# Optimization experiments

Hardware: AMD Instinct MI355X
Metric: run time of the kernel (lower is better)

The kernel has to match this reference:

```python
import jax, jax.numpy as jnp
import numpy as np
from jax import lax

SIZES = (32, 64, 128, 256, 512)
STRIDES = (4, 8, 16, 32, 64)
RATIOS = (0.5, 1.0, 2.0)
LVL_HW = ((256, 256), (128, 128), (64, 64), (32, 32), (16, 16))
IMG_H = IMG_W = 1024
NMS_T = 0.7
PRE_K = 6000   # pre_nms_topk[False]
POST_K = 1000  # post_nms_topk[False]
SCALE_CLAMP = float(np.log(1000.0 / 16))


def _anchors():
    """Detectron2-style anchors, one size per level, HWA ordering (anchor innermost)."""
    out = []
    for size, stride, (H, W) in zip(SIZES, STRIDES, LVL_HW):
        r = np.asarray(RATIOS, np.float64)
        ws = np.sqrt(size * size / r)
        hs = ws * r
        cell = np.stack([-ws / 2, -hs / 2, ws / 2, hs / 2], axis=1)  # [A,4]
        yy, xx = np.meshgrid(np.arange(H) * stride, np.arange(W) * stride, indexing='ij')
        shifts = np.stack([xx, yy, xx, yy], axis=-1).reshape(-1, 1, 4)  # [HW,1,4]
        out.append(jnp.asarray((shifts + cell[None]).reshape(-1, 4), jnp.float32))  # [HW*A,4]
    return out


def _conv(x, w, b, pad):
    y = lax.conv_general_dilated(x, w, (1, 1), [(pad, pad), (pad, pad)],
                                 dimension_numbers=('NCHW', 'OIHW', 'NCHW'))
    return y + b[None, :, None, None]


def _apply_deltas(deltas, anchors):
    # deltas [N,M,4], anchors [M,4]; Box2BoxTransform weights (1,1,1,1)
    w = anchors[:, 2] - anchors[:, 0]
    h = anchors[:, 3] - anchors[:, 1]
    cx = anchors[:, 0] + 0.5 * w
    cy = anchors[:, 1] + 0.5 * h
    dx, dy = deltas[..., 0], deltas[..., 1]
    dw = jnp.minimum(deltas[..., 2], SCALE_CLAMP)
    dh = jnp.minimum(deltas[..., 3], SCALE_CLAMP)
    pcx = dx * w + cx
    pcy = dy * h + cy
    pw = jnp.exp(dw) * w
    ph = jnp.exp(dh) * h
    return jnp.stack([pcx - 0.5 * pw, pcy - 0.5 * ph, pcx + 0.5 * pw, pcy + 0.5 * ph], -1)


def _nms(boxes, scores):
    """Fixed-iteration greedy NMS: boxes [M,4], scores [M] -> (idx [POST_K], valid [POST_K])."""
    areas = (boxes[:, 2] - boxes[:, 0]) * (boxes[:, 3] - boxes[:, 1])

    def body(s, _):
        i = jnp.argmax(s)
        bs = s[i]
        bb = boxes[i]
        x1 = jnp.maximum(bb[0], boxes[:, 0])
        y1 = jnp.maximum(bb[1], boxes[:, 1])
        x2 = jnp.minimum(bb[2], boxes[:, 2])
        y2 = jnp.minimum(bb[3], boxes[:, 3])
        inter = jnp.clip(x2 - x1, 0.0) * jnp.clip(y2 - y1, 0.0)
        iou = inter / (areas[i] + areas - inter + 1e-9)
        s2 = jnp.where(iou > NMS_T, -jnp.inf, s).at[i].set(-jnp.inf)
        return s2, (i, bs > -jnp.inf)

    _, (idx, valid) = lax.scan(body, scores, None, length=POST_K)
    return idx, valid


def setup_inputs() -> dict:
    key = jax.random.key(0)
    ks = jax.random.split(key, 8)
    C = 256
    inp = {}
    for i, (H, W) in enumerate(LVL_HW):
        inp[f'f{i + 2}'] = jax.random.normal(ks[i], (2, C, H, W), jnp.float32)
    inp['conv_w'] = 0.01 * jax.random.normal(ks[5], (C, C, 3, 3), jnp.float32)
    inp['conv_b'] = jnp.zeros((C,), jnp.float32)
    inp['obj_w'] = 0.01 * jax.random.normal(ks[6], (3, C, 1, 1), jnp.float32)
    inp['obj_b'] = jnp.zeros((3,), jnp.float32)
    inp['delta_w'] = 0.01 * jax.random.normal(ks[7], (12, C, 1, 1), jnp.float32)
    inp['delta_b'] = jnp.zeros((12,), jnp.float32)
    return inp


def reference(f2, f3, f4, f5, f6, conv_w, conv_b, obj_w, obj_b, delta_w, delta_b):
    feats = [f2, f3, f4, f5, f6]
    anchors = _anchors()

    logits_l, deltas_l = [], []
    for x in feats:
        t = jax.nn.relu(_conv(x, conv_w, conv_b, 1))
        lg = _conv(t, obj_w, obj_b, 0)        # [N,A,H,W]
        dl = _conv(t, delta_w, delta_b, 0)    # [N,A*4,H,W]
        N, A, H, W = lg.shape
        logits_l.append(lg.transpose(0, 2, 3, 1).reshape(N, -1))                       # [N,HWA]
        deltas_l.append(dl.reshape(N, A, 4, H, W).transpose(0, 3, 4, 1, 2).reshape(N, -1, 4))  # [N,HWA,4]

    combined = jnp.concatenate(
        [jnp.concatenate(logits_l, 1)[..., None], jnp.concatenate(deltas_l, 1)], -1)  # [N,Atot,5]

    # decode + per-level pre-NMS top-k
    cand_b, cand_s, cand_l = [], [], []
    for lvl, (lg, dl, an) in enumerate(zip(logits_l, deltas_l, anchors)):
        props = _apply_deltas(dl, an)          # [N,HWA,4]
        k = min(PRE_K, lg.shape[1])
        vals, idx = lax.top_k(lg, k)
        cand_b.append(jnp.take_along_axis(props, idx[..., None], 1))
        cand_s.append(vals)
        cand_l.append(jnp.full(vals.shape, float(lvl), jnp.float32))
    boxes = jnp.concatenate(cand_b, 1)   # [N,M,4]
    scores = jnp.concatenate(cand_s, 1)  # [N,M]
    lvl = jnp.concatenate(cand_l, 1)

    # clip to image
    boxes = jnp.stack([boxes[..., 0].clip(0, IMG_W), boxes[..., 1].clip(0, IMG_H),
                       boxes[..., 2].clip(0, IMG_W), boxes[..., 3].clip(0, IMG_H)], -1)
    # batched NMS via per-level coordinate offset (levels never overlap)
    off_boxes = boxes + (lvl * 2000.0)[..., None]
    idx, valid = jax.vmap(_nms)(off_boxes, scores)
    keep_boxes = jnp.take_along_axis(boxes, idx[..., None], 1)   # [N,POST_K,4]
    keep_scores = jnp.take_along_axis(scores, idx, 1)            # [N,POST_K]
    return combined, keep_boxes, keep_scores, valid
```

## Files before the change

kernel.cpp:

```cpp
#include <hip/hip_runtime.h>
#include <math.h>

#define ATOT 261888
#define MCAND 21840
#define POSTK 1000
#define CMB (2*ATOT*5)
#define KB_OFF CMB
#define KS_OFF (CMB+8000)
#define KV_OFF (CMB+10000)
#define SCALE_CLAMP 4.135166556742356f
#define RCAP 4096

typedef unsigned long long u64;

#define WS_T   0
#define WS_SC  (256*65536)
#define WS_CB  (WS_SC + 2*ATOT)
#define WS_CS  (WS_CB + 2*MCAND*4)
#define WS_CTL (WS_CS + 2*MCAND)

#define C_PRE 0
#define C_KCUR 6
#define C_CNT 12
#define C_TIE 18
#define N_THRPREV 24
#define N_KEPT 26
#define N_DONE 28
#define N_SCNT 30
#define N_LAST 32
#define C_GH 40
#define C_TIEIDX (C_GH + 6*256)
#define CTL_SIZE (C_TIEIDX + 6*1024)
#define WS_WP  (WS_CTL + CTL_SIZE)

#define FT_T   0
#define FT_TSZ 22347776
#define FT_SC  22347776
#define FT_CB  (FT_SC + 2*ATOT)
#define FT_CS  (FT_CB + 2*MCAND*4)
#define FT_CTL (FT_CS + 2*MCAND)
#define FT_WP  (FT_CTL + CTL_SIZE)
#define FT_END (FT_WP + 589824)

#define NS_KEY  0
#define NS_BOX  16384
#define NS_AREA 49152
#define NS_DIAG 57344
#define NS_PSUP 73728
#define NS_KBOX 73984
#define NS_MASK 84224

__device__ const int LW[5]    = {256,128,64,32,16};
__device__ const int LM[5]    = {196608,49152,12288,3072,768};
__device__ const int LBASE[5] = {0,196608,245760,258048,261120};
__device__ const int LSTR[5]  = {4,8,16,32,64};
__device__ const int LSZ[5]   = {32,64,128,256,512};
__device__ const int CBASE[5] = {0,6000,12000,18000,21072};
__device__ const int TOFF[5]  = {0,16777216,20971520,22020096,22282240};

__device__ inline unsigned fkey(float f) {
  unsigned u = __float_as_uint(f);
  return u ^ (unsigned)(((int)u >> 31) | 0x80000000);
}
__device__ inline float unfkey(unsigned k) {
  unsigned u = (k & 0x80000000u) ? (k ^ 0x80000000u) : ~k;
  return __uint_as_float(u);
}
__device__ inline int lvl_of(int idx) {
  return idx < 6000 ? 0 : idx < 12000 ? 1 : idx < 18000 ? 2 : idx < 21072 ? 3 : 4;
}
__device__ inline float iou_f(float ax1,float ay1,float ax2,float ay2,float aar,
                              float bx1,float by1,float bx2,float by2,float bar) {
  float ix1 = fmaxf(ax1,bx1), iy1 = fmaxf(ay1,by1);
  float ix2 = fminf(ax2,bx2), iy2 = fminf(ay2,by2);
  float inter = fmaxf(ix2-ix1,0.f) * fmaxf(iy2-iy1,0.f);
  return inter / (aar + bar - inter + 1e-9f);
}

typedef _Float16 f16;
typedef _Float16 f16x2 __attribute__((ext_vector_type(2)));
typedef _Float16 f16x8 __attribute__((ext_vector_type(8)));
typedef float f32x4 __attribute__((ext_vector_type(4)));

#define MFMA16(a,b,c) __builtin_amdgcn_mfma_f32_16x16x32_f16(a,b,c,0,0,0)
#define AST 40
#define WHALF 589824

__global__ __launch_bounds__(256) void wprep_mfma(const float* __restrict__ wgt,
                                                  f16* __restrict__ wsp) {
  int o = blockIdx.x*256 + threadIdx.x;
  if (o >= WHALF) return;
  int j  = o & 7;
  int oc = (o >> 3) & 255;
  int ks = (o >> 11) & 3;
  int kc = (o >> 13) & 7;
  int t  = o >> 16;
  int ci = kc*32 + ks*8 + j;
  float v = wgt[(oc*256 + ci)*9 + t] * 2048.f;
  f16 hi = (f16)v;
  f16 lo = (f16)(v - (float)hi);
  wsp[o] = hi;
  wsp[WHALF + o] = lo;
}

#define HALO 324
#define SBUF 25920

__global__ __launch_bounds__(512,2) void conv_big(
    const float* __restrict__ f0, const float* __restrict__ f1,
    const float* __restrict__ f2, const float* __restrict__ f3,
    const float* __restrict__ f4, const f16* __restrict__ wsp,
    const float* __restrict__ bias,
    const float* __restrict__ ow, const float* __restrict__ obp,
    const float* __restrict__ dwp, const float* __restrict__ dbp,
    float* __restrict__ comb, float* __restrict__ scores) {
  __shared__ __align__(16) char SBc[103680];
  __shared__ float wHs[15][256];
  const int tid = threadIdx.x;

  int id = blockIdx.x;
  int n = (id >= 341) ? 1 : 0;
  int rem = id - n*341;
  int lvl, tile;
  if (rem < 256)      { lvl = 0; tile = rem; }
  else if (rem < 320) { lvl = 1; tile = rem - 256; }
  else if (rem < 336) { lvl = 2; tile = rem - 320; }
  else if (rem < 340) { lvl = 3; tile = rem - 336; }
  else                { lvl = 4; tile = 0; }
  const int W = LW[lvl], H = W, HW = W*W;
  const int tw = W >> 4;
  const int ty0 = tile / tw, tx0 = tile - ty0*tw;
  const int x0 = tx0*16, y0 = ty0*16;
  const int lbase = LBASE[lvl];
  const float* in = (lvl==0?f0:lvl==1?f1:lvl==2?f2:lvl==3?f3:f4) + (long)n*256*HW;

  const int wv   = tid >> 6;
  const int lane = tid & 63;
  const int l15  = lane & 15;
  const int ks   = lane >> 4;
  const int rg   = wv >> 2;
  const int cg   = wv & 3;

  for (int i = tid; i < 768; i += 512)  wHs[i>>8][i&255] = ow[i];
  for (int i = tid; i < 3072; i += 512) wHs[3+(i>>8)][i&255] = dwp[i];

  auto stage = [&](int kc, int b) {
    f16* AhB = (f16*)SBc + b*SBUF;
    f16* AlB = AhB + 12960;
    float v0r[10], v1r[10];
    #pragma unroll
    for (int it = 0; it < 10; ++it) {
      int i = tid + it*512;
      int cp = i / HALO; int p = i - cp*HALO;
      int hy = p / 18, hx = p - hy*18;
      int gy = y0 + hy - 1, gx = x0 + hx - 1;
      int cy = min(max(gy, 0), H-1), cx = min(max(gx, 0), W-1);
      const float* q = in + (long)(kc*32 + 2*cp)*HW + cy*W + cx;
      v0r[it] = q[0];
      v1r[it] = q[HW];
    }
    #pragma unroll
    for (int it = 0; it < 10; ++it) {
      int i = tid + it*512;
      int cp = i / HALO; int p = i - cp*HALO;
      int hy = p / 18, hx = p - hy*18;
      int gy = y0 + hy - 1, gx = x0 + hx - 1;
      bool okb = (gy >= 0) & (gy < H) & (gx >= 0) & (gx < W);
      float v0 = okb ? v0r[it]*2048.f : 0.f;
      float v1 = okb ? v1r[it]*2048.f : 0.f;
      f16 h0 = (f16)v0, h1 = (f16)v1;
      f16 e0 = (f16)(v0 - (float)h0), e1 = (f16)(v1 - (float)h1);
      f16x2 ph; ph[0] = h0; ph[1] = h1;
      f16x2 pl; pl[0] = e0; pl[1] = e1;
      *(f16x2*)&AhB[p*AST + 2*cp] = ph;
      *(f16x2*)&AlB[p*AST + 2*cp] = pl;
    }
    if (tid < 64) {
      int p = 5120 + tid - 15*HALO;
      int hy = p / 18, hx = p - hy*18;
      int gy = y0 + hy - 1, gx = x0 + hx - 1;
      float v0 = 0.f, v1 = 0.f;
      if (gy >= 0 && gy < H && gx >= 0 && gx < W) {
        const float* q = in + (long)(kc*32 + 30)*HW + gy*W + gx;
        v0 = q[0]*2048.f; v1 = q[HW]*2048.f;
      }
      f16 h0 = (f16)v0, h1 = (f16)v1;
      f16 e0 = (f16)(v0 - (float)h0), e1 = (f16)(v1 - (float)h1);
      f16x2 ph; ph[0] = h0; ph[1] = h1;
      f16x2 pl; pl[0] = e0; pl[1] = e1;
      *(f16x2*)&AhB[p*AST + 30] = ph;
      *(f16x2*)&AlB[p*AST + 30] = pl;
    }
  };

  const f32x4 vzero = {0.f, 0.f, 0.f, 0.f};
  f32x4 acc[8][4];
  #pragma unroll
  for (int mt = 0; mt < 8; ++mt)
    #pragma unroll
    for (int nt = 0; nt < 4; ++nt) acc[mt][nt] = vzero;

  stage(0, 0);
  __syncthreads();

  for (int kc = 0; kc < 8; ++kc) {
    const int b = kc & 1;
    if (kc < 7) stage(kc + 1, b ^ 1);
    const f16* AhB = (const f16*)SBc + b*SBUF;
    const f16* AlB = AhB + 12960;
    for (int t = 0; t < 9; ++t) {
      const int tyk = t / 3, txk = t - (t/3)*3;
      const f16* wb = wsp + (((t*8 + kc)*4 + ks)*256 + cg*64 + l15)*8;
      f16x8 Bh0 = *(const f16x8*)(wb);
      f16x8 Bh1 = *(const f16x8*)(wb + 128);
      f16x8 Bh2 = *(const f16x8*)(wb + 256);
      f16x8 Bh3 = *(const f16x8*)(wb + 384);
      f16x8 Bl0 = *(const f16x8*)(wb + WHALF);
      f16x8 Bl1 = *(const f16x8*)(wb + WHALF + 128);
      f16x8 Bl2 = *(const f16x8*)(wb + WHALF + 256);
      f16x8 Bl3 = *(const f16x8*)(wb + WHALF + 384);
      #pragma unroll
      for (int mt = 0; mt < 8; ++mt) {
        const int p = (rg*8 + mt + tyk)*18 + l15 + txk;
        f16x8 Af = *(const f16x8*)&AhB[p*AST + ks*8];
        f16x8 Ae = *(const f16x8*)&AlB[p*AST + ks*8];
        acc[mt][0] = MFMA16(Af, Bh0, acc[mt][0]);
        acc[mt][1] = MFMA16(Af, Bh1, acc[mt][1]);
        acc[mt][2] = MFMA16(Af, Bh2, acc[mt][2]);
        acc[mt][3] = MFMA16(Af, Bh3, acc[mt][3]);
        acc[mt][0] = MFMA16(Ae, Bh0, acc[mt][0]);
        acc[mt][1] = MFMA16(Ae, Bh1, acc[mt][1]);
        acc[mt][2] = MFMA16(Ae, Bh2, acc[mt][2]);
        acc[mt][3] = MFMA16(Ae, Bh3, acc[mt][3]);
        acc[mt][0] = MFMA16(Af, Bl0, acc[mt][0]);
        acc[mt][1] = MFMA16(Af, Bl1, acc[mt][1]);
        acc[mt][2] = MFMA16(Af, Bl2, acc[mt][2]);
        acc[mt][3] = MFMA16(Af, Bl3, acc[mt][3]);
      }
    }
    __syncthreads();
  }

  const float rs = 1.f / 4194304.f;
  float* part = (float*)SBc;
  float bb[4];
  #pragma unroll
  for (int nt = 0; nt < 4; ++nt) bb[nt] = bias[cg*64 + nt*16 + l15];

  #pragma unroll
  for (int mt = 0; mt < 8; ++mt) {
    f32x4 y[4];
    #pragma unroll
    for (int nt = 0; nt < 4; ++nt) {
      f32x4 a = acc[mt][nt];
      y[nt][0] = fmaxf(a[0]*rs + bb[nt], 0.f);
      y[nt][1] = fmaxf(a[1]*rs + bb[nt], 0.f);
      y[nt][2] = fmaxf(a[2]*rs + bb[nt], 0.f);
      y[nt][3] = fmaxf(a[3]*rs + bb[nt], 0.f);
    }
    #pragma unroll
    for (int j = 0; j < 15; ++j) {
      float w0 = wHs[j][cg*64 + l15];
      float w1 = wHs[j][cg*64 + 16 + l15];
      float w2 = wHs[j][cg*64 + 32 + l15];
      float w3 = wHs[j][cg*64 + 48 + l15];
      f32x4 p4;
      p4[0] = y[0][0]*w0 + y[1][0]*w1 + y[2][0]*w2 + y[3][0]*w3;
      p4[1] = y[0][1]*w0 + y[1][1]*w1 + y[2][1]*w2 + y[3][1]*w3;
      p4[2] = y[0][2]*w0 + y[1][2]*w1 + y[2][2]*w2 + y[3][2]*w3;
      p4[3] = y[0][3]*w0 + y[1][3]*w1 + y[2][3]*w2 + y[3][3]*w3;
      #pragma unroll
      for (int m = 1; m < 16; m <<= 1) {
        p4[0] += __shfl_xor(p4[0], m);
        p4[1] += __shfl_xor(p4[1], m);
        p4[2] += __shfl_xor(p4[2], m);
        p4[3] += __shfl_xor(p4[3], m);
      }
      if (l15 == 0) {
        float* pp = part + ((((cg*2 + rg)*8 + mt)*4 + ks)*15 + j)*4;
        pp[0] = p4[0]; pp[1] = p4[1]; pp[2] = p4[2]; pp[3] = p4[3];
      }
    }
  }
  __syncthreads();
  if (tid < 256) {
    int rg2 = tid >> 7, mt = (tid >> 4) & 7, xi = tid & 15;
    int k2 = xi >> 2, xj = xi & 3;
    float v[15];
    #pragma unroll
    for (int j = 0; j < 15; ++j) {
      float s = 0.f;
      #pragma unroll
      for (int c2 = 0; c2 < 4; ++c2)
        s += part[((((c2*2 + rg2)*8 + mt)*4 + k2)*15 + j)*4 + xj];
      v[j] = s;
    }
    int pos = (y0 + rg2*8 + mt)*W + x0 + xi;
    long base = (long)n*ATOT + lbase + (long)pos*3;
    #pragma unroll
    for (int a = 0; a < 3; ++a) {
      float lg = v[a] + obp[a];
      comb[(base+a)*5] = lg;
      scores[(long)n*ATOT + lbase + pos*3 + a] = lg;
      #pragma unroll
      for (int q = 0; q < 4; ++q)
        comb[(base+a)*5 + 1 + q] = v[3 + a*4 + q] + dbp[a*4+q];
    }
  }
}

__global__ __launch_bounds__(256,2) void conv_lvl_mfma(
    const float* __restrict__ in, const f16* __restrict__ wsp,
    const float* __restrict__ bias, float* __restrict__ outp, int H, int W) {
  __shared__ __align__(16) char SBc[28800];
  f16* Ah = (f16*)SBc;
  f16* Al = (f16*)(SBc + 14400);
  const int tid  = threadIdx.x;
  const int wv   = tid >> 6;
  const int lane = tid & 63;
  const int l15  = lane & 15;
  const int ks   = lane >> 4;
  const int HW   = H * W;
  const int x0 = blockIdx.x*16, y0 = blockIdx.y*8;

  const f32x4 vzero = {0.f, 0.f, 0.f, 0.f};
  f32x4 acc[8][4];
  #pragma unroll
  for (int mt = 0; mt < 8; ++mt)
    #pragma unroll
    for (int nt = 0; nt < 4; ++nt) acc[mt][nt] = vzero;

  for (int kc = 0; kc < 8; ++kc) {
    __syncthreads();
    for (int i = tid; i < 2880; i += 256) {
      int cp = i / 180; int p = i - cp*180;
      int hy = p / 18, hx = p - hy*18;
      int gy = y0 + hy - 1, gx = x0 + hx - 1;
      float v0 = 0.f, v1 = 0.f;
      if (gy >= 0 && gy < H && gx >= 0 && gx < W) {
        const float* q = in + (long)(kc*32 + 2*cp)*HW + gy*W + gx;
        v0 = q[0] * 2048.f;
        v1 = q[HW] * 2048.f;
      }
      f16 h0 = (f16)v0, h1 = (f16)v1;
      f16 e0 = (f16)(v0 - (float)h0), e1 = (f16)(v1 - (float)h1);
      f16x2 ph; ph[0] = h0; ph[1] = h1;
      f16x2 pl; pl[0] = e0; pl[1] = e1;
      *(f16x2*)&Ah[p*AST + 2*cp] = ph;
      *(f16x2*)&Al[p*AST + 2*cp] = pl;
    }
    __syncthreads();
    for (int t = 0; t < 9; ++t) {
      const int tyk = t / 3, txk = t - (t/3)*3;
      const f16* wb = wsp + (((t*8 + kc)*4 + ks)*256 + wv*64 + l15)*8;
      f16x8 Bh0 = *(const f16x8*)(wb);
      f16x8 Bh1 = *(const f16x8*)(wb + 128);
      f16x8 Bh2 = *(const f16x8*)(wb + 256);
      f16x8 Bh3 = *(const f16x8*)(wb + 384);
      f16x8 Bl0 = *(const f16x8*)(wb + WHALF);
      f16x8 Bl1 = *(const f16x8*)(wb + WHALF + 128);
      f16x8 Bl2 = *(const f16x8*)(wb + WHALF + 256);
      f16x8 Bl3 = *(const f16x8*)(wb + WHALF + 384);
      #pragma unroll
      for (int mt = 0; mt < 8; ++mt) {
        const int p = (mt + tyk)*18 + l15 + txk;
        f16x8 Af = *(const f16x8*)&Ah[p*AST + ks*8];
        f16x8 Ae = *(const f16x8*)&Al[p*AST + ks*8];
        acc[mt][0] = MFMA16(Af, Bh0, acc[mt][0]);
        acc[mt][1] = MFMA16(Af, Bh1, acc[mt][1]);
        acc[mt][2] = MFMA16(Af, Bh2, acc[mt][2]);
        acc[mt][3] = MFMA16(Af, Bh3, acc[mt][3]);
        acc[mt][0] = MFMA16(Ae, Bh0, acc[mt][0]);
        acc[mt][1] = MFMA16(Ae, Bh1, acc[mt][1]);
        acc[mt][2] = MFMA16(Ae, Bh2, acc[mt][2]);
        acc[mt][3] = MFMA16(Ae, Bh3, acc[mt][3]);
        acc[mt][0] = MFMA16(Af, Bl0, acc[mt][0]);
        acc[mt][1] = MFMA16(Af, Bl1, acc[mt][1]);
        acc[mt][2] = MFMA16(Af, Bl2, acc[mt][2]);
        acc[mt][3] = MFMA16(Af, Bl3, acc[mt][3]);
      }
    }
  }
  const float rs = 1.f / 4194304.f;
  #pragma unroll
  for (int nt = 0; nt < 4; ++nt) {
    int oc = wv*64 + nt*16 + l15;
    float bbv = bias[oc];
    #pragma unroll
    for (int mt = 0; mt < 8; ++mt) {
      f32x4 a = acc[mt][nt];
      float4 v;
      v.x = fmaxf(a[0]*rs + bbv, 0.f);
      v.y = fmaxf(a[1]*rs + bbv, 0.f);
      v.z = fmaxf(a[2]*rs + bbv, 0.f);
      v.w = fmaxf(a[3]*rs + bbv, 0.f);
      *(float4*)&outp[(long)oc*HW + (y0+mt)*W + x0 + ks*4] = v;
    }
  }
}

__global__ __launch_bounds__(256) void heads1x1(
    const float* __restrict__ t, const float* __restrict__ ow, const float* __restrict__ ob,
    const float* __restrict__ dw, const float* __restrict__ db,
    float* __restrict__ comb, float* __restrict__ scores, int HW, int lbase, int n) {
  __shared__ float wS[15][256];
  const int tid = threadIdx.x;
  for (int i = tid; i < 3*256; i += 256) wS[i>>8][i&255] = ow[i];
  for (int i = tid; i < 12*256; i += 256) wS[3+(i>>8)][i&255] = dw[i];
  __syncthreads();
  int p0 = (blockIdx.x*256 + threadIdx.x)*4;
  if (p0 >= HW) return;
  float acc[15][4] = {};
  for (int c = 0; c < 256; ++c) {
    float4 v = *(const float4*)&t[c*HW + p0];
    float vv[4] = {v.x, v.y, v.z, v.w};
    #pragma unroll
    for (int k = 0; k < 15; ++k) {
      float w = wS[k][c];
      #pragma unroll
      for (int j = 0; j < 4; ++j) acc[k][j] += w * vv[j];
    }
  }
  float obv[3]; for (int i2 = 0; i2 < 3; ++i2) obv[i2] = ob[i2];
  float dbv[12]; for (int i2 = 0; i2 < 12; ++i2) dbv[i2] = db[i2];
  for (int j = 0; j < 4; ++j) {
    int pos = p0 + j;
    long base = (long)n*ATOT + lbase + (long)pos*3;
    #pragma unroll
    for (int a = 0; a < 3; ++a) {
      float lg = acc[a][j] + obv[a];
      comb[(base+a)*5] = lg;
      scores[(long)n*ATOT + lbase + pos*3 + a] = lg;
      #pragma unroll
      for (int q = 0; q < 4; ++q)
        comb[(base+a)*5 + 1 + q] = acc[3 + a*4 + q][j] + dbv[a*4+q];
    }
  }
}

__device__ void decode_store(int n, int lvl, int idx, int slot,
                             const float* comb, float* cboxes, float* cscores) {
  int W = LW[lvl];
  int a = idx % 3; int p = idx / 3;
  int wx = p % W, hy = p / W;
  double r = (a == 0) ? 0.5 : (a == 1) ? 1.0 : 2.0;
  double sz = (double)LSZ[lvl];
  double wsd = sqrt(sz*sz/r);
  double hsd = wsd * r;
  double cxd = (double)(wx * LSTR[lvl]);
  double cyd = (double)(hy * LSTR[lvl]);
  float ax1 = (float)(cxd - 0.5*wsd), ay1 = (float)(cyd - 0.5*hsd);
  float ax2 = (float)(cxd + 0.5*wsd), ay2 = (float)(cyd + 0.5*hsd);
  float aw = ax2 - ax1, ah = ay2 - ay1;
  float acx = ax1 + 0.5f*aw, acy = ay1 + 0.5f*ah;
  long g = (long)n*ATOT + LBASE[lvl] + idx;
  const float* cm = comb + g*5;
  float sc = cm[0];
  float dx = cm[1], dy = cm[2], dwv = cm[3], dhv = cm[4];
  dwv = fminf(dwv, SCALE_CLAMP); dhv = fminf(dhv, SCALE_CLAMP);
  float pcx = __fadd_rn(__fmul_rn(dx, aw), acx);
// ... 253 lines not shown
    }
  }
}

__global__ __launch_bounds__(64) void nms_scan(
    const float* __restrict__ cscores, const float* __restrict__ cboxes,
    float* __restrict__ wt, unsigned* ctl, float* __restrict__ dout) {
  const int n = blockIdx.x;
  if (ctl[N_DONE + n]) return;
  const int lane = threadIdx.x;
  const float* cb = cboxes + (long)n*MCAND*4;
  u64* skeyG = ((u64*)(wt + NS_KEY)) + n*RCAP;
  const float* boxO  = wt + NS_BOX + n*RCAP*4;
  const float* areaG = wt + NS_AREA + n*RCAP;
  u64* mask  = ((u64*)(wt + NS_MASK)) + (long)n*RCAP*64;
  u64* diagA = ((u64*)(wt + NS_DIAG)) + n*64*64;
  u64* psupW = ((u64*)(wt + NS_PSUP)) + n*64;
  float* kbox = wt + NS_KBOX + n*1024*5;
  float* keepB = dout + KB_OFF + (long)n*4*POSTK;
  float* keepS = dout + KS_OFF + (long)n*POSTK;
  float* keepV = dout + KV_OFF + (long)n*POSTK;
  int scnt = (int)ctl[N_SCNT + n];
  int kt = (int)ctl[N_KEPT + n];
  __shared__ u64 alive[64];
  {
    int rem = scnt - lane*64;
    u64 a = rem >= 64 ? ~0ull : (rem > 0 ? ((1ull << rem) - 1ull) : 0ull);
    alive[lane] = a & ~psupW[lane];
  }
  __syncthreads();
  for (int c = 0; c < 64 && kt < POSTK; ++c) {
    u64 w64 = alive[c];
    if (!w64) continue;
    u64 diag = diagA[c*64 + lane];
    u64 kb = 0;
    while (w64) {
      int b = __ffsll(w64) - 1;
      kb |= (1ull << b);
      w64 &= ~(1ull << b);
      u64 sup = __shfl(diag, b);
      w64 &= ~sup;
      if (++kt >= POSTK) break;
    }
    alive[c] = 0;
    if ((kb >> lane) & 1) {
      int base = kt - (int)__popcll(kb);
      int pos = base + (int)__popcll(kb & ((1ull << lane) - 1ull));
      int s = c*64 + lane;
      u64 v = skeyG[s];
      int idx = (int)(~(unsigned)v);
      keepB[pos*4+0]=cb[idx*4+0]; keepB[pos*4+1]=cb[idx*4+1];
      keepB[pos*4+2]=cb[idx*4+2]; keepB[pos*4+3]=cb[idx*4+3];
      keepS[pos] = unfkey((unsigned)(v >> 32));
      keepV[pos] = 1.f;
      kbox[pos*5+0]=boxO[s*4+0]; kbox[pos*5+1]=boxO[s*4+1];
      kbox[pos*5+2]=boxO[s*4+2]; kbox[pos*5+3]=boxO[s*4+3];
      kbox[pos*5+4]=areaG[s];
    }
    __syncthreads();
    if (kb && lane > c && alive[lane]) {
      u64 acc = 0, m = kb;
      while (m) {
        int b = __ffsll(m) - 1; m &= m - 1;
        acc |= mask[(long)(c*64 + b)*64 + lane];
      }
      if (acc) alive[lane] &= ~acc;
    }
    __syncthreads();
  }
  if (lane == 0) {
    ctl[N_KEPT + n] = (unsigned)kt;
    if (kt >= POSTK || ctl[N_LAST + n]) ctl[N_DONE + n] = 1;
  }
}

__device__ inline u64 shfl_down_u64d(u64 v, int o) {
  unsigned hi = __shfl_down((unsigned)(v >> 32), o);
  unsigned lo = __shfl_down((unsigned)v, o);
  return ((u64)hi << 32) | lo;
}
__global__ __launch_bounds__(1024) void nms_fill(
    const float* __restrict__ cscores, const float* __restrict__ cboxes,
    unsigned* ctl, float* __restrict__ dout) {
  const int n = blockIdx.x;
  const int tid = threadIdx.x;
  const int lane = tid & 63;
  const int wid = tid >> 6;
  const float* sc = cscores + (long)n*MCAND;
  const float* cb = cboxes + (long)n*MCAND*4;
  float* keepB = dout + KB_OFF + (long)n*4*POSTK;
  float* keepS = dout + KS_OFF + (long)n*POSTK;
  float* keepV = dout + KV_OFF + (long)n*POSTK;
  __shared__ u64 wred[16];
  __shared__ u64 sBest;
  u64 best = 0;
  for (int i = tid; i < 6000; i += 1024) {
    u64 v = ((u64)fkey(sc[i]) << 32) | (unsigned)(~i);
    if (v > best) best = v;
  }
  for (int o = 32; o > 0; o >>= 1) {
    u64 ov = shfl_down_u64d(best, o);
    if (ov > best) best = ov;
  }
  if (lane == 0) wred[wid] = best;
  __syncthreads();
  if (tid == 0) {
    u64 b = 0;
    for (int i = 0; i < 16; ++i) if (wred[i] > b) b = wred[i];
    sBest = b;
  }
  __syncthreads();
  int kt = (int)ctl[N_KEPT + n];
  int bidx = (int)(~(unsigned)sBest);
  float b0 = cb[bidx*4+0], b1 = cb[bidx*4+1], b2 = cb[bidx*4+2], b3 = cb[bidx*4+3];
  float bsc = sc[bidx];
  for (int s2 = kt + tid; s2 < POSTK; s2 += 1024) {
    keepB[s2*4+0]=b0; keepB[s2*4+1]=b1; keepB[s2*4+2]=b2; keepB[s2*4+3]=b3;
    keepS[s2] = bsc; keepV[s2] = 0.f;
  }
}

extern "C" void kernel_launch(void* const* d_in, const int* in_sizes, int n_in,
                              void* d_out, int out_size, void* d_ws, size_t ws_size,
                              hipStream_t stream) {
  const float* feats[5];
  for (int i = 0; i < 5; ++i) feats[i] = (const float*)d_in[i];
  const float* conv_w  = (const float*)d_in[5];
  const float* conv_b  = (const float*)d_in[6];
  const float* obj_w   = (const float*)d_in[7];
  const float* obj_b   = (const float*)d_in[8];
  const float* delta_w = (const float*)d_in[9];
  const float* delta_b = (const float*)d_in[10];
  float* out = (float*)d_out;
  float* ws = (float*)d_ws;

  const bool big = ws_size >= (size_t)FT_END * 4ull;
  float *t, *scores, *cboxes, *cscores, *wp;
  unsigned* ctl;
  if (big) {
    t = ws + FT_T; scores = ws + FT_SC; cboxes = ws + FT_CB;
    cscores = ws + FT_CS; ctl = (unsigned*)(ws + FT_CTL); wp = ws + FT_WP;
  } else {
    t = ws + WS_T; scores = ws + WS_SC; cboxes = ws + WS_CB;
    cscores = ws + WS_CS; ctl = (unsigned*)(ws + WS_CTL); wp = ws + WS_WP;
  }

  static const int LWh[5]    = {256,128,64,32,16};
  static const int LBASEh[5] = {0,196608,245760,258048,261120};

  wprep_mfma<<<dim3(2304), dim3(256), 0, stream>>>(conv_w, (f16*)wp);
  init_ctl<<<dim3(1), dim3(256), 0, stream>>>(ctl);

  if (big) {
    conv_big<<<dim3(682), dim3(512), 0, stream>>>(
        feats[0], feats[1], feats[2], feats[3], feats[4], (const f16*)wp, conv_b,
        obj_w, obj_b, delta_w, delta_b, out, scores);
  } else {
    for (int n = 0; n < 2; ++n) {
      for (int lvl = 0; lvl < 5; ++lvl) {
        int H = LWh[lvl], W = LWh[lvl], HW = H*W;
        conv_lvl_mfma<<<dim3(W/16, H/8), dim3(256), 0, stream>>>(
            feats[lvl] + (long)n*256*HW, (const f16*)wp, conv_b, t, H, W);
        int hb = (HW + 1023) / 1024;
        heads1x1<<<dim3(hb), dim3(256), 0, stream>>>(
            t, obj_w, obj_b, delta_w, delta_b, out, scores, HW, LBASEh[lvl], n);
      }
    }
  }

  for (int p = 0; p < 4; ++p) {
    tk_hist<<<dim3(48,6), dim3(256), 0, stream>>>(scores, ctl, p);
    tk_pick<<<dim3(6), dim3(256), 0, stream>>>(ctl);
  }
  tk_compact<<<dim3(48,6), dim3(256), 0, stream>>>(scores, out, ctl, cboxes, cscores);
  tk_finalize<<<dim3(6), dim3(64), 0, stream>>>(out, ctl, cboxes, cscores);
  decode34<<<dim3(15,2), dim3(256), 0, stream>>>(out, cboxes, cscores);
  for (int b = 0; b < 6; ++b) {
    nms_select<<<dim3(2), dim3(1024), 0, stream>>>(cscores, cboxes, t, ctl);
    nms_matrix<<<dim3(64,2), dim3(256), 0, stream>>>(t, t, ctl);
    nms_scan<<<dim3(2), dim3(64), 0, stream>>>(cscores, cboxes, t, ctl, out);
  }
  nms_fill<<<dim3(2), dim3(1024), 0, stream>>>(cscores, cboxes, ctl, out);
}
```

Baseline: 1.656 ms.

## Widen conv_big to 1024 threads with channel-major LDS layout and deferred stage writes

Result: slower. 5.308 ms (+220.6%).

```diff
diff --git a/kernel.cpp b/kernel.cpp
--- a/kernel.cpp
+++ b/kernel.cpp
@@ -103,10 +103,11 @@
   wsp[WHALF + o] = lo;
 }
 
-#define HALO 324
-#define SBUF 25920
-
-__global__ __launch_bounds__(512,2) void conv_big(
+#define NUNIT 1296
+#define ABUF 10368
+#define SBUF2 20736
+
+__global__ __launch_bounds__(1024,4) void conv_big(
     const float* __restrict__ f0, const float* __restrict__ f1,
     const float* __restrict__ f2, const float* __restrict__ f3,
     const float* __restrict__ f4, const f16* __restrict__ wsp,
@@ -114,7 +115,7 @@
     const float* __restrict__ ow, const float* __restrict__ obp,
     const float* __restrict__ dwp, const float* __restrict__ dbp,
     float* __restrict__ comb, float* __restrict__ scores) {
-  __shared__ __align__(16) char SBc[103680];
+  __shared__ __align__(16) char SBc[82944];
   __shared__ float wHs[15][256];
   const int tid = threadIdx.x;
 
@@ -138,174 +139,164 @@
   const int lane = tid & 63;
   const int l15  = lane & 15;
   const int ks   = lane >> 4;
-  const int rg   = wv >> 2;
-  const int cg   = wv & 3;
-
-  for (int i = tid; i < 768; i += 512)  wHs[i>>8][i&255] = ow[i];
-  for (int i = tid; i < 3072; i += 512) wHs[3+(i>>8)][i&255] = dwp[i];
-
-  auto stage = [&](int kc, int b) {
-    f16* AhB = (f16*)SBc + b*SBUF;
-    f16* AlB = AhB + 12960;
-    float v0r[10], v1r[10];
+  const int rg   = wv >> 3;
+  const int cg   = wv & 7;
+
+  for (int i = tid; i < 768; i += 1024)  wHs[i>>8][i&255] = ow[i];
+  for (int i = tid; i < 3072; i += 1024) wHs[3+(i>>8)][i&255] = dwp[i];
+
+  int ks0 = tid / 324; int p0 = tid - ks0*324;
+  int hy0 = p0/18, hx0 = p0 - hy0*18;
+  int gy0 = y0 + hy0 - 1, gx0 = x0 + hx0 - 1;
+  const bool okb0 = (gy0>=0) & (gy0<H) & (gx0>=0) & (gx0<W);
+  const int boff0 = ks0*8*HW + min(max(gy0,0),H-1)*W + min(max(gx0,0),W-1);
+  const bool has1 = tid < 272;
+  int p1 = tid + 52;
+  int hy1 = p1/18, hx1 = p1 - hy1*18;
+  int gy1 = y0 + hy1 - 1, gx1 = x0 + hx1 - 1;
+  const bool okb1 = (gy1>=0) & (gy1<H) & (gx1>=0) & (gx1<W);
+  const int boff1 = 24*HW + min(max(gy1,0),H-1)*W + min(max(gx1,0),W-1);
+
+  float sv0[8], sv1[8];
+  auto stage_load = [&](int kc) {
+    const float* q = in + (size_t)(kc*32)*HW;
     #pragma unroll
-    for (int it = 0; it < 10; ++it) {
-      int i = tid + it*512;
-      int cp = i / HALO; int p = i - cp*HALO;
-      int hy = p / 18, hx = p - hy*18;
-      int gy = y0 + hy - 1, gx = x0 + hx - 1;
-      int cy = min(max(gy, 0), H-1), cx = min(max(gx, 0), W-1);
-      const float* q = in + (long)(kc*32 + 2*cp)*HW + cy*W + cx;
-      v0r[it] = q[0];
-      v1r[it] = q[HW];
-    }
+    for (int j = 0; j < 8; ++j) sv0[j] = q[boff0 + j*HW];
+    if (has1) {
+      #pragma unroll
+      for (int j = 0; j < 8; ++j) sv1[j] = q[boff1 + j*HW];
+    }
+  };
+  auto stage_write = [&](int b) {
+    f16* AhB = (f16*)SBc + b*SBUF2;
+    f16* AlB = AhB + ABUF;
+    f16x8 vh, vl;
     #pragma unroll
-    for (int it = 0; it < 10; ++it) {
-      int i = tid + it*512;
-      int cp = i / HALO; int p = i - cp*HALO;
-      int hy = p / 18, hx = p - hy*18;
-      int gy = y0 + hy - 1, gx = x0 + hx - 1;
-      bool okb = (gy >= 0) & (gy < H) & (gx >= 0) & (gx < W);
-      float v0 = okb ? v0r[it]*2048.f : 0.f;
-      float v1 = okb ? v1r[it]*2048.f : 0.f;
-      f16 h0 = (f16)v0, h1 = (f16)v1;
-      f16 e0 = (f16)(v0 - (float)h0), e1 = (f16)(v1 - (float)h1);
-      f16x2 ph; ph[0] = h0; ph[1] = h1;
-      f16x2 pl; pl[0] = e0; pl[1] = e1;
-      *(f16x2*)&AhB[p*AST + 2*cp] = ph;
-      *(f16x2*)&AlB[p*AST + 2*cp] = pl;
-    }
-    if (tid < 64) {
-      int p = 5120 + tid - 15*HALO;
-      int hy = p / 18, hx = p - hy*18;
-      int gy = y0 + hy - 1, gx = x0 + hx - 1;
-      float v0 = 0.f, v1 = 0.f;
-      if (gy >= 0 && gy < H && gx >= 0 && gx < W) {
-        const float* q = in + (long)(kc*32 + 30)*HW + gy*W + gx;
-        v0 = q[0]*2048.f; v1 = q[HW]*2048.f;
-      }
-      f16 h0 = (f16)v0, h1 = (f16)v1;
-      f16 e0 = (f16)(v0 - (float)h0), e1 = (f16)(v1 - (float)h1);
-      f16x2 ph; ph[0] = h0; ph[1] = h1;
-      f16x2 pl; pl[0] = e0; pl[1] = e1;
-      *(f16x2*)&AhB[p*AST + 30] = ph;
-      *(f16x2*)&AlB[p*AST + 30] = pl;
+    for (int j = 0; j < 8; ++j) {
+      float v = okb0 ? sv0[j]*2048.f : 0.f;
+      f16 h = (f16)v; vh[j] = h; vl[j] = (f16)(v - (float)h);
+    }
+    *(f16x8*)&AhB[tid*8] = vh;
+    *(f16x8*)&AlB[tid*8] = vl;
+    if (has1) {
+      #pragma unroll
+      for (int j = 0; j < 8; ++j) {
+        float v = okb1 ? sv1[j]*2048.f : 0.f;
+        f16 h = (f16)v; vh[j] = h; vl[j] = (f16)(v - (float)h);
+      }
+      *(f16x8*)&AhB[(1024+tid)*8] = vh;
+      *(f16x8*)&AlB[(1024+tid)*8] = vl;
     }
   };
 
   const f32x4 vzero = {0.f, 0.f, 0.f, 0.f};
-  f32x4 acc[8][4];
+  f32x4 acc[8][2];
   #pragma unroll
-  for (int mt = 0; mt < 8; ++mt)
-    #pragma unroll
-    for (int nt = 0; nt < 4; ++nt) acc[mt][nt] = vzero;
-
-  stage(0, 0);
+  for (int mt = 0; mt < 8; ++mt) { acc[mt][0] = vzero; acc[mt][1] = vzero; }
+
+  stage_load(0);
+  stage_write(0);
   __syncthreads();
 
   for (int kc = 0; kc < 8; ++kc) {
     const int b = kc & 1;
-    if (kc < 7) stage(kc + 1, b ^ 1);
-    const f16* AhB = (const f16*)SBc + b*SBUF;
-    const f16* AlB = AhB + 12960;
+    if (kc < 7) stage_load(kc + 1);
+    const f16* AhB = (const f16*)SBc + b*SBUF2;
+    const f16* AlB = AhB + ABUF;
     for (int t = 0; t < 9; ++t) {
       const int tyk = t / 3, txk = t - (t/3)*3;
-      const f16* wb = wsp + (((t*8 + kc)*4 + ks)*256 + cg*64 + l15)*8;
+      const f16* wb = wsp + (((t*8 + kc)*4 + ks)*256 + cg*32 + l15)*8;
       f16x8 Bh0 = *(const f16x8*)(wb);
       f16x8 Bh1 = *(const f16x8*)(wb + 128);
-      f16x8 Bh2 = *(const f16x8*)(wb + 256);
-      f16x8 Bh3 = *(const f16x8*)(wb + 384);
       f16x8 Bl0 = *(const f16x8*)(wb + WHALF);
       f16x8 Bl1 = *(const f16x8*)(wb + WHALF + 128);
-      f16x8 Bl2 = *(const f16x8*)(wb + WHALF + 256);
-      f16x8 Bl3 = *(const f16x8*)(wb + WHALF + 384);
       #pragma unroll
       for (int mt = 0; mt < 8; ++mt) {
         const int p = (rg*8 + mt + tyk)*18 + l15 + txk;
-        f16x8 Af = *(const f16x8*)&AhB[p*AST + ks*8];
-        f16x8 Ae = *(const f16x8*)&AlB[p*AST + ks*8];
+        f16x8 Af = *(const f16x8*)&AhB[(ks*324 + p)*8];
+        f16x8 Ae = *(const f16x8*)&AlB[(ks*324 + p)*8];
         acc[mt][0] = MFMA16(Af, Bh0, acc[mt][0]);
         acc[mt][1] = MFMA16(Af, Bh1, acc[mt][1]);
-        acc[mt][2] = MFMA16(Af, Bh2, acc[mt][2]);
-        acc[mt][3] = MFMA16(Af, Bh3, acc[mt][3]);
         acc[mt][0] = MFMA16(Ae, Bh0, acc[mt][0]);
         acc[mt][1] = MFMA16(Ae, Bh1, acc[mt][1]);
-        acc[mt][2] = MFMA16(Ae, Bh2, acc[mt][2]);
-        acc[mt][3] = MFMA16(Ae, Bh3, acc[mt][3]);
         acc[mt][0] = MFMA16(Af, Bl0, acc[mt][0]);
         acc[mt][1] = MFMA16(Af, Bl1, acc[mt][1]);
-        acc[mt][2] = MFMA16(Af, Bl2, acc[mt][2]);
-        acc[mt][3] = MFMA16(Af, Bl3, acc[mt][3]);
-      }
-    }
+      }
+    }
+    if (kc < 7) stage_write(b ^ 1);
     __syncthreads();
   }
 
   const float rs = 1.f / 4194304.f;
-  float* part = (float*)SBc;
-  float bb[4];
-  #pragma unroll
-  for (int nt = 0; nt < 4; ++nt) bb[nt] = bias[cg*64 + nt*16 + l15];
-
+  float bb0 = bias[cg*32 + l15], bb1 = bias[cg*32 + 16 + l15];
   #pragma unroll
   for (int mt = 0; mt < 8; ++mt) {
-    f32x4 y[4];
+    f32x4 a0 = acc[mt][0], a1 = acc[mt][1];
     #pragma unroll
-    for (int nt = 0; nt < 4; ++nt) {
-      f32x4 a = acc[mt][nt];
-      y[nt][0] = fmaxf(a[0]*rs + bb[nt], 0.f);
-      y[nt][1] = fmaxf(a[1]*rs + bb[nt], 0.f);
-      y[nt][2] = fmaxf(a[2]*rs + bb[nt], 0.f);
-      y[nt][3] = fmaxf(a[3]*rs + bb[nt], 0.f);
-    }
+    for (int i = 0; i < 4; ++i) {
+      a0[i] = fmaxf(a0[i]*rs + bb0, 0.f);
+      a1[i] = fmaxf(a1[i]*rs + bb1, 0.f);
+    }
+    acc[mt][0] = a0; acc[mt][1] = a1;
+  }
+
+  float* part = (float*)SBc;
+  #pragma unroll
+  for (int h = 0; h < 2; ++h) {
+    const int jb = h*8;
     #pragma unroll
-    for (int j = 0; j < 15; ++j) {
-      float w0 = wHs[j][cg*64 + l15];
-      float w1 = wHs[j][cg*64 + 16 + l15];
-      float w2 = wHs[j][cg*64 + 32 + l15];
-      float w3 = wHs[j][cg*64 + 48 + l15];
-      f32x4 p4;
-      p4[0] = y[0][0]*w0 + y[1][0]*w1 + y[2][0]*w2 + y[3][0]*w3;
-      p4[1] = y[0][1]*w0 + y[1][1]*w1 + y[2][1]*w2 + y[3][1]*w3;
-      p4[2] = y[0][2]*w0 + y[1][2]*w1 + y[2][2]*w2 + y[3][2]*w3;
-      p4[3] = y[0][3]*w0 + y[1][3]*w1 + y[2][3]*w2 + y[3][3]*w3;
+    for (int mt = 0; mt < 8; ++mt) {
       #pragma unroll
-      for (int m = 1; m < 16; m <<= 1) {
-        p4[0] += __shfl_xor(p4[0], m);
-        p4[1] += __shfl_xor(p4[1], m);
-        p4[2] += __shfl_xor(p4[2], m);
-        p4[3] += __shfl_xor(p4[3], m);
-      }
-      if (l15 == 0) {
-        float* pp = part + ((((cg*2 + rg)*8 + mt)*4 + ks)*15 + j)*4;
-        pp[0] = p4[0]; pp[1] = p4[1]; pp[2] = p4[2]; pp[3] = p4[3];
-      }
-    }
-  }
-  __syncthreads();
-  if (tid < 256) {
-    int rg2 = tid >> 7, mt = (tid >> 4) & 7, xi = tid & 15;
-    int k2 = xi >> 2, xj = xi & 3;
-    float v[15];
-    #pragma unroll
-    for (int j = 0; j < 15; ++j) {
-      float s = 0.f;
+      for (int jj = 0; jj < 8; ++jj) {
+        const int j = jb + jj;
+        if (j < 15) {
+          float w0 = wHs[j][cg*32 + l15];
+          float w1 = wHs[j][cg*32 + 16 + l15];
+          f32x4 p4;
+          #pragma unroll
+          for (int i = 0; i < 4; ++i)
+            p4[i] = acc[mt][0][i]*w0 + acc[mt][1][i]*w1;
+          #pragma unroll
+          for (int m = 1; m < 16; m <<= 1) {
+            p4[0] += __shfl_xor(p4[0], m);
+            p4[1] += __shfl_xor(p4[1], m);
+            p4[2] += __shfl_xor(p4[2], m);
+            p4[3] += __shfl_xor(p4[3], m);
+          }
+          if (l15 == 0) {
+            float* pp = part + ((((cg*2 + rg)*8 + mt)*4 + ks)*8 + jj)*4;
+            pp[0] = p4[0]; pp[1] = p4[1]; pp[2] = p4[2]; pp[3] = p4[3];
+          }
+        }
+      }
+    }
+    __syncthreads();
+    if (tid < 256) {
+      int row16 = tid >> 4, xi = tid & 15;
+      int rg2 = row16 >> 3, mt = row16 & 7;
+      int k2 = xi >> 2, xj = xi & 3;
+      int pos = (y0 + rg2*8 + mt)*W + x0 + xi;
+      long base = (long)n*ATOT + lbase + (long)pos*3;
       #pragma unroll
-      for (int c2 = 0; c2 < 4; ++c2)
-        s += part[((((c2*2 + rg2)*8 + mt)*4 + k2)*15 + j)*4 + xj];
-      v[j] = s;
-    }
-    int pos = (y0 + rg2*8 + mt)*W + x0 + xi;
-    long base = (long)n*ATOT + lbase + (long)pos*3;
-    #pragma unroll
-    for (int a = 0; a < 3; ++a) {
-      float lg = v[a] + obp[a];
-      comb[(base+a)*5] = lg;
-      scores[(long)n*ATOT + lbase + pos*3 + a] = lg;
-      #pragma unroll
-      for (int q = 0; q < 4; ++q)
-        comb[(base+a)*5 + 1 + q] = v[3 + a*4 + q] + dbp[a*4+q];
-    }
+      for (int jj = 0; jj < 8; ++jj) {
+        const int j = jb + jj;
+        if (j < 15) {
+          float s = 0.f;
+          #pragma unroll
+          for (int c2 = 0; c2 < 8; ++c2)
+            s += part[((((c2*2 + rg2)*8 + mt)*4 + k2)*8 + jj)*4 + xj];
+          if (j < 3) {
+            float lg = s + obp[j];
+            comb[(base+j)*5] = lg;
+            scores[(long)n*ATOT + lbase + pos*3 + j] = lg;
+          } else {
+            int a = (j-3) >> 2, q = (j-3) & 3;
+            comb[(base+a)*5 + 1 + q] = s + dbp[j-3];
+          }
+        }
+      }
+    }
+    __syncthreads();
   }
 }
 
@@ -865,7 +856,7 @@
   init_ctl<<<dim3(1), dim3(256), 0, stream>>>(ctl);
 
   if (big) {
-    conv_big<<<dim3(682), dim3(512), 0, stream>>>(
+    conv_big<<<dim3(682), dim3(1024), 0, stream>>>(
         feats[0], feats[1], feats[2], feats[3], feats[4], (const f16*)wp, conv_b,
         obj_w, obj_b, delta_w, delta_b, out, scores);
   } else {
```

## Restructure conv input staging into k-slice-major LDS layout with precomputed offsets

Applied to the files above, without the earlier changes.

New measurement: 1.640 ms. No clear change (-0.9%).

```diff
diff --git a/kernel.cpp b/kernel.cpp
--- a/kernel.cpp
+++ b/kernel.cpp
@@ -103,8 +103,8 @@
   wsp[WHALF + o] = lo;
 }
 
-#define HALO 324
-#define SBUF 25920
+#define ABUF2 10368
+#define SBUF2 20736
 
 __global__ __launch_bounds__(512,2) void conv_big(
     const float* __restrict__ f0, const float* __restrict__ f1,
@@ -114,7 +114,7 @@
     const float* __restrict__ ow, const float* __restrict__ obp,
     const float* __restrict__ dwp, const float* __restrict__ dbp,
     float* __restrict__ comb, float* __restrict__ scores) {
-  __shared__ __align__(16) char SBc[103680];
+  __shared__ __align__(16) char SBc[82944];
   __shared__ float wHs[15][256];
   const int tid = threadIdx.x;
 
@@ -144,52 +144,69 @@
   for (int i = tid; i < 768; i += 512)  wHs[i>>8][i&255] = ow[i];
   for (int i = tid; i < 3072; i += 512) wHs[3+(i>>8)][i&255] = dwp[i];
 
+  int ubo0, ubo1, ubo2; bool uin0, uin1, uin2;
+  {
+    int u = tid;
+    int ksu = u / 324, pu = u - ksu*324;
+    int hy = pu/18, hx = pu - hy*18;
+    int gy = y0 + hy - 1, gx = x0 + hx - 1;
+    uin0 = (gy>=0) & (gy<H) & (gx>=0) & (gx<W);
+    ubo0 = ksu*8*HW + min(max(gy,0),H-1)*W + min(max(gx,0),W-1);
+  }
+  {
+    int u = tid + 512;
+    int ksu = u / 324, pu = u - ksu*324;
+    int hy = pu/18, hx = pu - hy*18;
+    int gy = y0 + hy - 1, gx = x0 + hx - 1;
+    uin1 = (gy>=0) & (gy<H) & (gx>=0) & (gx<W);
+    ubo1 = ksu*8*HW + min(max(gy,0),H-1)*W + min(max(gx,0),W-1);
+  }
+  const bool has2 = tid < 272;
+  {
+    int u = has2 ? tid + 1024 : 0;
+    int ksu = u / 324, pu = u - ksu*324;
+    int hy = pu/18, hx = pu - hy*18;
+    int gy = y0 + hy - 1, gx = x0 + hx - 1;
+    uin2 = (gy>=0) & (gy<H) & (gx>=0) & (gx<W);
+    ubo2 = ksu*8*HW + min(max(gy,0),H-1)*W + min(max(gx,0),W-1);
+  }
+
+  float sv0[8], sv1[8], sv2[8];
   auto stage = [&](int kc, int b) {
-    f16* AhB = (f16*)SBc + b*SBUF;
-    f16* AlB = AhB + 12960;
-    float v0r[10], v1r[10];
-    #pragma unroll
-    for (int it = 0; it < 10; ++it) {
-      int i = tid + it*512;
-      int cp = i / HALO; int p = i - cp*HALO;
-      int hy = p / 18, hx = p - hy*18;
-      int gy = y0 + hy - 1, gx = x0 + hx - 1;
-      int cy = min(max(gy, 0), H-1), cx = min(max(gx, 0), W-1);
-      const float* q = in + (long)(kc*32 + 2*cp)*HW + cy*W + cx;
-      v0r[it] = q[0];
-      v1r[it] = q[HW];
-    }
-    #pragma unroll
-    for (int it = 0; it < 10; ++it) {
-      int i = tid + it*512;
-      int cp = i / HALO; int p = i - cp*HALO;
-      int hy = p / 18, hx = p - hy*18;
-      int gy = y0 + hy - 1, gx = x0 + hx - 1;
-      bool okb = (gy >= 0) & (gy < H) & (gx >= 0) & (gx < W);
-      float v0 = okb ? v0r[it]*2048.f : 0.f;
-      float v1 = okb ? v1r[it]*2048.f : 0.f;
-      f16 h0 = (f16)v0, h1 = (f16)v1;
-      f16 e0 = (f16)(v0 - (float)h0), e1 = (f16)(v1 - (float)h1);
-      f16x2 ph; ph[0] = h0; ph[1] = h1;
-      f16x2 pl; pl[0] = e0; pl[1] = e1;
-      *(f16x2*)&AhB[p*AST + 2*cp] = ph;
-      *(f16x2*)&AlB[p*AST + 2*cp] = pl;
-    }
-    if (tid < 64) {
-      int p = 5120 + tid - 15*HALO;
-      int hy = p / 18, hx = p - hy*18;
-      int gy = y0 + hy - 1, gx = x0 + hx - 1;
-      float v0 = 0.f, v1 = 0.f;
-      if (gy >= 0 && gy < H && gx >= 0 && gx < W) {
-        const float* q = in + (long)(kc*32 + 30)*HW + gy*W + gx;
-        v0 = q[0]*2048.f; v1 = q[HW]*2048.f;
-      }
-      f16 h0 = (f16)v0, h1 = (f16)v1;
-      f16 e0 = (f16)(v0 - (float)h0), e1 = (f16)(v1 - (float)h1);
-      f16x2 ph; ph[0] = h0; ph[1] = h1;
-      f16x2 pl; pl[0] = e0; pl[1] = e1;
-      *(f16x2*)&AhB[p*AST + 30] = ph;
-      *(f16x2*)&AlB[p*AST + 30] = pl;
+    const float* q = in + (size_t)(kc*32)*HW;
+    #pragma unroll
+    for (int j = 0; j < 8; ++j) sv0[j] = q[ubo0 + j*HW];
+    #pragma unroll
+    for (int j = 0; j < 8; ++j) sv1[j] = q[ubo1 + j*HW];
+    if (has2) {
+      #pragma unroll
+      for (int j = 0; j < 8; ++j) sv2[j] = q[ubo2 + j*HW];
+    }
+    f16* AhB = (f16*)SBc + b*SBUF2;
+    f16* AlB = AhB + ABUF2;
+    f16x8 vh, vl;
+    #pragma unroll
+    for (int j = 0; j < 8; ++j) {
+      float v = uin0 ? sv0[j]*2048.f : 0.f;
+      f16 h = (f16)v; vh[j] = h; vl[j] = (f16)(v - (float)h);
+    }
+    *(f16x8*)&AhB[tid*8] = vh;
+    *(f16x8*)&AlB[tid*8] = vl;
+    #pragma unroll
+    for (int j = 0; j < 8; ++j) {
+      float v = uin1 ? sv1[j]*2048.f : 0.f;
+      f16 h = (f16)v; vh[j] = h; vl[j] = (f16)(v - (float)h);
+    }
+    *(f16x8*)&AhB[(tid+512)*8] = vh;
+    *(f16x8*)&AlB[(tid+512)*8] = vl;
+    if (has2) {
+      #pragma unroll
+      for (int j = 0; j < 8; ++j) {
+        float v = uin2 ? sv2[j]*2048.f : 0.f;
+        f16 h = (f16)v; vh[j] = h; vl[j] = (f16)(v - (float)h);
+      }
+      *(f16x8*)&AhB[(tid+1024)*8] = vh;
+      *(f16x8*)&AlB[(tid+1024)*8] = vl;
     }
   };
 
@@ -206,8 +223,8 @@
   for (int kc = 0; kc < 8; ++kc) {
     const int b = kc & 1;
     if (kc < 7) stage(kc + 1, b ^ 1);
-    const f16* AhB = (const f16*)SBc + b*SBUF;
-    const f16* AlB = AhB + 12960;
+    const f16* AhB = (const f16*)SBc + b*SBUF2;
+    const f16* AlB = AhB + ABUF2;
     for (int t = 0; t < 9; ++t) {
       const int tyk = t / 3, txk = t - (t/3)*3;
       const f16* wb = wsp + (((t*8 + kc)*4 + ks)*256 + cg*64 + l15)*8;
@@ -222,8 +239,8 @@
       #pragma unroll
       for (int mt = 0; mt < 8; ++mt) {
         const int p = (rg*8 + mt + tyk)*18 + l15 + txk;
-        f16x8 Af = *(const f16x8*)&AhB[p*AST + ks*8];
-        f16x8 Ae = *(const f16x8*)&AlB[p*AST + ks*8];
+        f16x8 Af = *(const f16x8*)&AhB[(ks*324 + p)*8];
+        f16x8 Ae = *(const f16x8*)&AlB[(ks*324 + p)*8];
         acc[mt][0] = MFMA16(Af, Bh0, acc[mt][0]);
         acc[mt][1] = MFMA16(Af, Bh1, acc[mt][1]);
         acc[mt][2] = MFMA16(Af, Bh2, acc[mt][2]);
```
